# Kernel optimization log

Hardware: AMD Instinct MI355X
Metric: run time of the kernel (lower is better)

## Reference

```python
import jax, jax.numpy as jnp
import numpy as np

E = 8        # num_experts
D = 512      # embed_size
H = 8        # attention heads
HD = D // H  # head dim
B, S = 4, 1024


def setup_inputs() -> dict:
    key = jax.random.key(0)
    ks = jax.random.split(key, 16)
    sd = 0.02
    return {
        "x":  jax.random.normal(ks[0], (B, S, D), jnp.float32),
        # per-expert FFN params, stacked over expert dim
        "W1": jax.random.normal(ks[1], (E, D, 4 * D), jnp.float32) * sd,
        "b1": jnp.zeros((E, 4 * D), jnp.float32),
        "W2": jax.random.normal(ks[2], (E, 4 * D, D), jnp.float32) * sd,
        "b2": jnp.zeros((E, D), jnp.float32),
        # MultiheadAttention in_proj (split) and out_proj
        "Wq": jax.random.normal(ks[3], (D, D), jnp.float32) * sd,
        "bq": jnp.zeros((D,), jnp.float32),
        "Wk": jax.random.normal(ks[4], (D, D), jnp.float32) * sd,
        "bk": jnp.zeros((D,), jnp.float32),
        "Wv": jax.random.normal(ks[5], (D, D), jnp.float32) * sd,
        "bv": jnp.zeros((D,), jnp.float32),
        "Wo": jax.random.normal(ks[6], (D, D), jnp.float32) * sd,
        "bo": jnp.zeros((D,), jnp.float32),
        "expert_id": 3,
    }


def reference(x, W1, b1, W2, b2, Wq, bq, Wk, bk, Wv, bv, Wo, bo, expert_id):
    # --- batched per-expert FFN (fuses the Python loop over experts) ---
    # hidden: [B, E, S, 4D]
    hidden = jax.nn.relu(jnp.einsum('bsd,edf->besf', x, W1) + b1[None, :, None, :])
    eo = jnp.einsum('besf,efd->besd', hidden, W2) + b2[None, :, None, :]  # [B,E,S,D]
    eo = eo.transpose(0, 2, 1, 3)  # [B, S, E, D]

    Bs, Ss = x.shape[0], x.shape[1]
    a = eo.reshape(Bs * Ss, E, D)  # [N, E, D]; attention runs over the expert dim

    # --- MultiheadAttention (batch_first), torch semantics ---
    # NOTE: the original passes a FLOAT tril-of-ones attn_mask, which torch ADDS
    # to the scores (it does NOT mask with -inf). We reproduce that faithfully.
    q = (a @ Wq.T + bq).reshape(-1, E, H, HD).transpose(0, 2, 1, 3)  # [N,H,E,hd]
    k = (a @ Wk.T + bk).reshape(-1, E, H, HD).transpose(0, 2, 1, 3)
    v = (a @ Wv.T + bv).reshape(-1, E, H, HD).transpose(0, 2, 1, 3)

    mask = jnp.tril(jnp.ones((E, E), jnp.float32))  # additive float mask
    scores = jnp.einsum('nhed,nhfd->nhef', q, k) / jnp.sqrt(jnp.float32(HD))
    scores = scores + mask[None, None, :, :]
    attn = jax.nn.softmax(scores, axis=-1)
    ctx = jnp.einsum('nhef,nhfd->nhed', attn, v)           # [N,H,E,hd]
    ctx = ctx.transpose(0, 2, 1, 3).reshape(-1, E, D)       # [N,E,D]
    out = ctx @ Wo.T + bo                                   # [N,E,D]

    out = out.reshape(Bs, Ss, E, D)
    return out[:, :, expert_id, :]  # [B, S, D]
```

## Files before the change

kernel.cpp:

```cpp
#include <hip/hip_runtime.h>
#include <hip/hip_bf16.h>

typedef __hip_bfloat16 bf16;
typedef __attribute__((ext_vector_type(4))) float f32x4;
typedef __attribute__((ext_vector_type(8))) short s16x8;

#define N_TOK 4096
#define Dm    512
#define Fm    2048
#define Em    8

__device__ __forceinline__ float bf2f(bf16 v) { return __bfloat162float(v); }
__device__ __forceinline__ bf16  f2bf(float f) { return __float2bfloat16(f); }

#define GL16(g, l)                                                              \
  __builtin_amdgcn_global_load_lds(                                             \
      (const __attribute__((address_space(1))) void*)(g),                       \
      (__attribute__((address_space(3))) void*)(l), 16, 0, 0)

__global__ void cvt_f32_bf16(const float* __restrict__ in, bf16* __restrict__ out, int n4) {
  int i = blockIdx.x * 256 + threadIdx.x;
  if (i >= n4) return;
  float4 v = reinterpret_cast<const float4*>(in)[i];
  bf16 tmp[4] = {f2bf(v.x), f2bf(v.y), f2bf(v.z), f2bf(v.w)};
  __builtin_memcpy(out + (size_t)i * 4, tmp, 8);
}

__global__ void transpose_cvt(const float* __restrict__ in, bf16* __restrict__ out,
                              int R, int C, long inb, long outb) {
  in  += (long)blockIdx.z * inb;
  out += (long)blockIdx.z * outb;
  __shared__ float t[32][33];
  int tx = threadIdx.x & 31, ty = threadIdx.x >> 5;
  int c0 = blockIdx.x * 32, r0 = blockIdx.y * 32;
#pragma unroll
  for (int i = 0; i < 32; i += 8)
    t[ty + i][tx] = in[(long)(r0 + ty + i) * C + c0 + tx];
  __syncthreads();
#pragma unroll
  for (int i = 0; i < 32; i += 8)
    out[(long)(c0 + ty + i) * R + r0 + tx] = f2bf(t[tx][ty + i]);
}

template <bool RELU, bool OUT_BF16>
__global__ __launch_bounds__(256, 2) void gemm_bt(
    const bf16* __restrict__ A, const bf16* __restrict__ Bt, void* __restrict__ Cout,
    const float* __restrict__ bias, int M, int N, int K, int lda, int ldb, int ldc,
    long abs_, long bbs, long cbs, long biasbs, const int* __restrict__ eid,
    int eid_scale) {
  int e = blockIdx.z;
  A    += (long)e * abs_;
  Bt   += (long)e * bbs;
  bias += (long)e * biasbs;
  long coff = (long)e * cbs;
  if (eid) A += (long)(*eid) * eid_scale;

  __shared__ bf16 As[128 * 32];
  __shared__ bf16 Bs[128 * 32];

  int tid = threadIdx.x;
  int wave = tid >> 6, lane = tid & 63;
  int wm = wave >> 1, wn = wave & 1;
  int bm = blockIdx.x * 128, bn = blockIdx.y * 128;

  int srow  = lane >> 2;
  int skoff = (lane & 3) * 8;

  f32x4 acc[4][4] = {};

  const bf16* Abase = A + (long)bm * lda;
  const bf16* Bbase = Bt + (long)bn * ldb;

  for (int k0 = 0; k0 < K; k0 += 32) {
    __syncthreads();
#pragma unroll
    for (int i = 0; i < 2; i++) {
      int r = wave * 32 + i * 16 + srow;
      GL16(Abase + (long)r * lda + k0 + skoff, As + (wave * 32 + i * 16) * 32);
      GL16(Bbase + (long)r * ldb + k0 + skoff, Bs + (wave * 32 + i * 16) * 32);
    }
    __syncthreads();

    s16x8 af[4], bfr[4];
#pragma unroll
    for (int m = 0; m < 4; m++)
      af[m] = *reinterpret_cast<const s16x8*>(As + (wm * 64 + m * 16 + (lane & 15)) * 32 +
                                              (lane >> 4) * 8);
#pragma unroll
    for (int n = 0; n < 4; n++)
      bfr[n] = *reinterpret_cast<const s16x8*>(Bs + (wn * 64 + n * 16 + (lane & 15)) * 32 +
                                               (lane >> 4) * 8);
#pragma unroll
    for (int m = 0; m < 4; m++)
#pragma unroll
      for (int n = 0; n < 4; n++)
        acc[m][n] = __builtin_amdgcn_mfma_f32_16x16x32_bf16(af[m], bfr[n], acc[m][n], 0, 0, 0);
  }

  int cr = (lane >> 4) * 4, cc = lane & 15;
#pragma unroll
  for (int m = 0; m < 4; m++) {
#pragma unroll
    for (int n = 0; n < 4; n++) {
      int col  = bn + wn * 64 + n * 16 + cc;
      float bv = bias ? bias[col] : 0.0f;
#pragma unroll
      for (int r = 0; r < 4; r++) {
        int row = bm + wm * 64 + m * 16 + cr + r;
        float v = acc[m][n][r] + bv;
        if (RELU) v = fmaxf(v, 0.0f);
        long idx = coff + (long)row * ldc + col;
        if (OUT_BF16)
          ((bf16*)Cout)[idx] = f2bf(v);
        else
          ((float*)Cout)[idx] = v;
      }
    }
  }
}

__global__ __launch_bounds__(256) void attn_kernel(const float* __restrict__ q,
                                                   const bf16* __restrict__ kv,
                                                   bf16* __restrict__ ctx,
                                                   const int* __restrict__ eid) {
  int wave = threadIdx.x >> 6, lane = threadIdx.x & 63;
  int n = blockIdx.x * 4 + wave;
  int h = lane >> 3, f = lane & 7;
  int e3 = *eid;
  const bf16* kvn = kv + (long)n * Em * (2 * Dm);
  const float* qh = q + (long)n * Dm + h * 64;
  const bf16* kf = kvn + f * (2 * Dm) + h * 64;
  float s = 0.f;
#pragma unroll
  for (int j = 0; j < 64; j++) s += qh[j] * bf2f(kf[j]);
  s *= 0.125f;
  s += (f <= e3) ? 1.0f : 0.0f;
  float mx = s;
#pragma unroll
  for (int d = 1; d < 8; d <<= 1) mx = fmaxf(mx, __shfl_xor(mx, d));
  float ex = expf(s - mx);
  float sm = ex;
#pragma unroll
  for (int d = 1; d < 8; d <<= 1) sm += __shfl_xor(sm, d);
  float at = ex / sm;
  int g = f;
  float acc[8] = {0, 0, 0, 0, 0, 0, 0, 0};
#pragma unroll
  for (int f2 = 0; f2 < 8; f2++) {
    float a = __shfl(at, (h << 3) | f2);
    const bf16* vf = kvn + f2 * (2 * Dm) + Dm + h * 64 + g * 8;
#pragma unroll
    for (int j = 0; j < 8; j++) acc[j] += a * bf2f(vf[j]);
  }
  bf16 tmp[8];
#pragma unroll
  for (int j = 0; j < 8; j++) tmp[j] = f2bf(acc[j]);
  __builtin_memcpy(ctx + (long)n * Dm + h * 64 + g * 8, tmp, 16);
}

extern "C" void kernel_launch(void* const* d_in, const int* in_sizes, int n_in,
                              void* d_out, int out_size, void* d_ws, size_t ws_size,
                              hipStream_t stream) {
  const float* x  = (const float*)d_in[0];
  const float* W1 = (const float*)d_in[1];
  const float* b1 = (const float*)d_in[2];
  const float* W2 = (const float*)d_in[3];
  const float* b2 = (const float*)d_in[4];
  const float* Wq = (const float*)d_in[5];
  const float* bq = (const float*)d_in[6];
  const float* Wk = (const float*)d_in[7];
  const float* bk = (const float*)d_in[8];
  const float* Wv = (const float*)d_in[9];
  const float* bv = (const float*)d_in[10];
  const float* Wo = (const float*)d_in[11];
  const float* bo = (const float*)d_in[12];
  const int* eid  = (const int*)d_in[13];

  char* w = (char*)d_ws;
  auto alloc = [&](size_t bytes) {
    char* p = w;
    w += (bytes + 255) & ~(size_t)255;
    return p;
  };
  bf16* xb   = (bf16*)alloc((size_t)N_TOK * Dm * 2);
  bf16* W1t  = (bf16*)alloc((size_t)Em * Fm * Dm * 2);
  bf16* W2t  = (bf16*)alloc((size_t)Em * Dm * Fm * 2);
  bf16* qw   = (bf16*)alloc((size_t)Dm * Dm * 2);
  bf16* kvw  = (bf16*)alloc((size_t)2 * Dm * Dm * 2);
  bf16* ow   = (bf16*)alloc((size_t)Dm * Dm * 2);
  float* bkv = (float*)alloc((size_t)2 * Dm * 4);
  bf16* hid  = (bf16*)alloc((size_t)Em * N_TOK * Fm * 2);
  bf16* eo   = (bf16*)alloc((size_t)N_TOK * Em * Dm * 2);
  bf16* kv   = (bf16*)hid;
  float* qb  = (float*)(hid + (size_t)N_TOK * Em * 2 * Dm);
  bf16* ctxb = (bf16*)(qb + (size_t)N_TOK * Dm);

  cvt_f32_bf16<<<(N_TOK * Dm / 4 + 255) / 256, 256, 0, stream>>>(x, xb, N_TOK * Dm / 4);
  transpose_cvt<<<dim3(Fm / 32, Dm / 32, Em), 256, 0, stream>>>(
      W1, W1t, Dm, Fm, (long)Dm * Fm, (long)Fm * Dm);
  transpose_cvt<<<dim3(Dm / 32, Fm / 32, Em), 256, 0, stream>>>(
      W2, W2t, Fm, Dm, (long)Fm * Dm, (long)Dm * Fm);
  int nw4 = Dm * Dm / 4;
  cvt_f32_bf16<<<(nw4 + 255) / 256, 256, 0, stream>>>(Wq, qw, nw4);
  cvt_f32_bf16<<<(nw4 + 255) / 256, 256, 0, stream>>>(Wk, kvw, nw4);
  cvt_f32_bf16<<<(nw4 + 255) / 256, 256, 0, stream>>>(Wv, kvw + (size_t)Dm * Dm, nw4);
  cvt_f32_bf16<<<(nw4 + 255) / 256, 256, 0, stream>>>(Wo, ow, nw4);
  hipMemcpyAsync(bkv, bk, Dm * sizeof(float), hipMemcpyDeviceToDevice, stream);
  hipMemcpyAsync(bkv + Dm, bv, Dm * sizeof(float), hipMemcpyDeviceToDevice, stream);

  gemm_bt<true, true><<<dim3(N_TOK / 128, Fm / 128, Em), 256, 0, stream>>>(
      xb, W1t, hid, b1, N_TOK, Fm, Dm, Dm, Dm, Fm,
      0L, (long)Fm * Dm, (long)N_TOK * Fm, (long)Fm, nullptr, 0);
  gemm_bt<false, true><<<dim3(N_TOK / 128, Dm / 128, Em), 256, 0, stream>>>(
      hid, W2t, eo, b2, N_TOK, Dm, Fm, Fm, Fm, Em * Dm,
      (long)N_TOK * Fm, (long)Dm * Fm, (long)Dm, (long)Dm, nullptr, 0);
  gemm_bt<false, true><<<dim3(N_TOK * Em / 128, 2 * Dm / 128, 1), 256, 0, stream>>>(
      eo, kvw, kv, bkv, N_TOK * Em, 2 * Dm, Dm, Dm, Dm, 2 * Dm,
      0L, 0L, 0L, 0L, nullptr, 0);
  gemm_bt<false, false><<<dim3(N_TOK / 128, Dm / 128, 1), 256, 0, stream>>>(
      eo, qw, qb, bq, N_TOK, Dm, Dm, Em * Dm, Dm, Dm,
      0L, 0L, 0L, 0L, eid, Dm);
  attn_kernel<<<N_TOK / 4, 256, 0, stream>>>(qb, kv, ctxb, eid);
  gemm_bt<false, false><<<dim3(N_TOK / 128, Dm / 128, 1), 256, 0, stream>>>(
      ctxb, ow, (float*)d_out, bo, N_TOK, Dm, Dm, Dm, Dm, Dm,
      0L, 0L, 0L, 0L, nullptr, 0);
}
```

Before: 314.4 us.

## Add 256x256 triple-buffered GEMM with swizzled LDS and XCD-aware block mapping

```diff
diff --git a/kernel.cpp b/kernel.cpp
--- a/kernel.cpp
+++ b/kernel.cpp
@@ -40,6 +40,122 @@
 #pragma unroll
   for (int i = 0; i < 32; i += 8)
     out[(long)(c0 + ty + i) * R + r0 + tx] = f2bf(t[tx][ty + i]);
+}
+
+template <bool RELU, bool OUT_BF16>
+__global__ __launch_bounds__(512, 2) void gemm256(
+    const bf16* __restrict__ A, const bf16* __restrict__ Bt, void* __restrict__ Cout,
+    const float* __restrict__ bias, int K, int lda, int ldb, int ldc,
+    long abs_, long bbs, long cbs, long biasbs, int gx, int gy) {
+  extern __shared__ bf16 lds[];
+
+  int nwg = gridDim.x;
+  int id  = blockIdx.x;
+  int lid = (id & 7) * (nwg >> 3) + (id >> 3);
+  int per = gx * gy;
+  int e   = lid / per;
+  int rem = lid - e * per;
+  int bx  = rem % gx, by = rem / gx;
+  int bm  = bx * 256, bn = by * 256;
+
+  A    += (long)e * abs_;
+  Bt   += (long)e * bbs;
+  bias += (long)e * biasbs;
+  long coff = (long)e * cbs;
+
+  int tid  = threadIdx.x;
+  int w    = tid >> 6, lane = tid & 63;
+  int wm   = w >> 2, wn = w & 3;
+
+  int srow   = lane >> 2;
+  int schunk = (lane & 3) ^ ((lane >> 3) & 3);
+
+  const bf16* Ab = A + (long)bm * lda;
+  const bf16* Bb = Bt + (long)bn * ldb;
+
+  int nt = K >> 5;
+
+  auto issue = [&](int t) {
+    int k0 = t << 5;
+    bf16* buf = lds + (t % 3) * 16384;
+#pragma unroll
+    for (int j = 0; j < 2; ++j) {
+      int ch   = j * 8 + w;
+      int rowA = ch * 16 + srow;
+      GL16(Ab + (long)rowA * lda + k0 + schunk * 8, buf + ch * 512);
+      GL16(Bb + (long)rowA * ldb + k0 + schunk * 8, buf + 8192 + ch * 512);
+    }
+  };
+
+  f32x4 acc[8][4] = {};
+  int la = lane & 15, q = lane >> 4;
+  int slotr = q ^ ((la >> 1) & 3);
+
+  auto compute = [&](int t) {
+    const bf16* Abuf = lds + (t % 3) * 16384;
+    const bf16* Bbuf = Abuf + 8192;
+    s16x8 af[8], bfr[4];
+#pragma unroll
+    for (int m = 0; m < 8; ++m) {
+      int r = wm * 128 + m * 16 + la;
+      af[m] = *reinterpret_cast<const s16x8*>(Abuf + r * 32 + slotr * 8);
+    }
+#pragma unroll
+    for (int n = 0; n < 4; ++n) {
+      int r = wn * 64 + n * 16 + la;
+      bfr[n] = *reinterpret_cast<const s16x8*>(Bbuf + r * 32 + slotr * 8);
+    }
+    __builtin_amdgcn_s_setprio(1);
+#pragma unroll
+    for (int m = 0; m < 8; ++m)
+#pragma unroll
+      for (int n = 0; n < 4; ++n)
+        acc[m][n] = __builtin_amdgcn_mfma_f32_16x16x32_bf16(bfr[n], af[m], acc[m][n], 0, 0, 0);
+    __builtin_amdgcn_s_setprio(0);
+  };
+
+  issue(0);
+  issue(1);
+
+  for (int t = 0; t < nt - 1; ++t) {
+    asm volatile("s_waitcnt vmcnt(4)" ::: "memory");
+    __builtin_amdgcn_s_barrier();
+    asm volatile("" ::: "memory");
+    __builtin_amdgcn_sched_barrier(0);
+    if (t + 2 < nt) issue(t + 2);
+    compute(t);
+    __builtin_amdgcn_sched_barrier(0);
+  }
+  asm volatile("s_waitcnt vmcnt(0)" ::: "memory");
+  __builtin_amdgcn_s_barrier();
+  asm volatile("" ::: "memory");
+  __builtin_amdgcn_sched_barrier(0);
+  compute(nt - 1);
+
+  int nbase0 = bn + wn * 64 + q * 4;
+#pragma unroll
+  for (int m = 0; m < 8; ++m) {
+    int gm = bm + wm * 128 + m * 16 + la;
+#pragma unroll
+    for (int n = 0; n < 4; ++n) {
+      int gn = nbase0 + n * 16;
+      float4 b4 = *reinterpret_cast<const float4*>(bias + gn);
+      float v0 = acc[m][n][0] + b4.x, v1 = acc[m][n][1] + b4.y;
+      float v2 = acc[m][n][2] + b4.z, v3 = acc[m][n][3] + b4.w;
+      if (RELU) {
+        v0 = fmaxf(v0, 0.f); v1 = fmaxf(v1, 0.f);
+        v2 = fmaxf(v2, 0.f); v3 = fmaxf(v3, 0.f);
+      }
+      long idx = coff + (long)gm * ldc + gn;
+      if (OUT_BF16) {
+        bf16 tmp[4] = {f2bf(v0), f2bf(v1), f2bf(v2), f2bf(v3)};
+        __builtin_memcpy((bf16*)Cout + idx, tmp, 8);
+      } else {
+        float tmp[4] = {v0, v1, v2, v3};
+        __builtin_memcpy((float*)Cout + idx, tmp, 16);
+      }
+    }
+  }
 }
 
 template <bool RELU, bool OUT_BF16>
@@ -195,6 +311,11 @@
   float* qb  = (float*)(hid + (size_t)N_TOK * Em * 2 * Dm);
   bf16* ctxb = (bf16*)(qb + (size_t)N_TOK * Dm);
 
+  hipFuncSetAttribute(reinterpret_cast<const void*>(gemm256<true, true>),
+                      hipFuncAttributeMaxDynamicSharedMemorySize, 98304);
+  hipFuncSetAttribute(reinterpret_cast<const void*>(gemm256<false, true>),
+                      hipFuncAttributeMaxDynamicSharedMemorySize, 98304);
+
   cvt_f32_bf16<<<(N_TOK * Dm / 4 + 255) / 256, 256, 0, stream>>>(x, xb, N_TOK * Dm / 4);
   transpose_cvt<<<dim3(Fm / 32, Dm / 32, Em), 256, 0, stream>>>(
       W1, W1t, Dm, Fm, (long)Dm * Fm, (long)Fm * Dm);
@@ -208,15 +329,15 @@
   hipMemcpyAsync(bkv, bk, Dm * sizeof(float), hipMemcpyDeviceToDevice, stream);
   hipMemcpyAsync(bkv + Dm, bv, Dm * sizeof(float), hipMemcpyDeviceToDevice, stream);
 
-  gemm_bt<true, true><<<dim3(N_TOK / 128, Fm / 128, Em), 256, 0, stream>>>(
-      xb, W1t, hid, b1, N_TOK, Fm, Dm, Dm, Dm, Fm,
-      0L, (long)Fm * Dm, (long)N_TOK * Fm, (long)Fm, nullptr, 0);
-  gemm_bt<false, true><<<dim3(N_TOK / 128, Dm / 128, Em), 256, 0, stream>>>(
-      hid, W2t, eo, b2, N_TOK, Dm, Fm, Fm, Fm, Em * Dm,
-      (long)N_TOK * Fm, (long)Dm * Fm, (long)Dm, (long)Dm, nullptr, 0);
-  gemm_bt<false, true><<<dim3(N_TOK * Em / 128, 2 * Dm / 128, 1), 256, 0, stream>>>(
-      eo, kvw, kv, bkv, N_TOK * Em, 2 * Dm, Dm, Dm, Dm, 2 * Dm,
-      0L, 0L, 0L, 0L, nullptr, 0);
+  gemm256<true, true><<<16 * 8 * Em, 512, 98304, stream>>>(
+      xb, W1t, hid, b1, Dm, Dm, Dm, Fm,
+      0L, (long)Fm * Dm, (long)N_TOK * Fm, (long)Fm, 16, 8);
+  gemm256<false, true><<<16 * 2 * Em, 512, 98304, stream>>>(
+      hid, W2t, eo, b2, Fm, Fm, Fm, Em * Dm,
+      (long)N_TOK * Fm, (long)Dm * Fm, (long)Dm, (long)Dm, 16, 2);
+  gemm256<false, true><<<128 * 4, 512, 98304, stream>>>(
+      eo, kvw, kv, bkv, Dm, Dm, Dm, 2 * Dm,
+      0L, 0L, 0L, 0L, 128, 4);
   gemm_bt<false, false><<<dim3(N_TOK / 128, Dm / 128, 1), 256, 0, stream>>>(
       eo, qw, qb, bq, N_TOK, Dm, Dm, Em * Dm, Dm, Dm,
       0L, 0L, 0L, 0L, eid, Dm);
```

Result: slower. 321.6 us (+2.3%).

## Add swizzled BK=64 GEMM with XCD-aware block remap for FFN and KV projections

Applied to the files above, without the earlier changes.

```diff
diff --git a/kernel.cpp b/kernel.cpp
--- a/kernel.cpp
+++ b/kernel.cpp
@@ -40,6 +40,94 @@
 #pragma unroll
   for (int i = 0; i < 32; i += 8)
     out[(long)(c0 + ty + i) * R + r0 + tx] = f2bf(t[tx][ty + i]);
+}
+
+template <bool RELU, bool OUT_BF16>
+__global__ __launch_bounds__(256, 4) void gemm128(
+    const bf16* __restrict__ A, const bf16* __restrict__ Bt, void* __restrict__ Cout,
+    const float* __restrict__ bias, int K, int lda, int ldb, int ldc,
+    long abs_, long bbs, long cbs, long biasbs, int gx, int gy,
+    const int* __restrict__ eid, int eid_scale) {
+  __shared__ bf16 As[128 * 64];
+  __shared__ bf16 Bs[128 * 64];
+
+  int nwg = gridDim.x;
+  int id  = blockIdx.x;
+  int lid = (id & 7) * (nwg >> 3) + (id >> 3);
+  int per = gx * gy;
+  int e   = lid / per;
+  int rem = lid - e * per;
+  int bx  = rem % gx, by = rem / gx;
+  int bm  = bx * 128, bn = by * 128;
+
+  A    += (long)e * abs_;
+  Bt   += (long)e * bbs;
+  bias += (long)e * biasbs;
+  long coff = (long)e * cbs;
+  if (eid) A += (long)(*eid) * eid_scale;
+
+  int tid = threadIdx.x, wv = tid >> 6, lane = tid & 63;
+  int wm = wv >> 1, wn = wv & 1;
+
+  const bf16* Ab = A + (long)bm * lda;
+  const bf16* Bb = Bt + (long)bn * ldb;
+
+  f32x4 acc[4][4] = {};
+  int la = lane & 15, q = lane >> 4;
+  int srow_lo = lane >> 3;
+
+  for (int k0 = 0; k0 < K; k0 += 64) {
+    __syncthreads();
+#pragma unroll
+    for (int j = 0; j < 4; ++j) {
+      int r = (wv * 4 + j) * 8 + srow_lo;
+      int c = (lane & 7) ^ (r & 7);
+      GL16(Ab + (long)r * lda + k0 + c * 8, As + (wv * 4 + j) * 512);
+      GL16(Bb + (long)r * ldb + k0 + c * 8, Bs + (wv * 4 + j) * 512);
+    }
+    __syncthreads();
+
+#pragma unroll
+    for (int kk = 0; kk < 2; ++kk) {
+      int ps = (kk * 4 + q) ^ (la & 7);
+      s16x8 af[4], bfr[4];
+#pragma unroll
+      for (int m = 0; m < 4; ++m)
+        af[m] = *reinterpret_cast<const s16x8*>(As + (wm * 64 + m * 16 + la) * 64 + ps * 8);
+#pragma unroll
+      for (int n = 0; n < 4; ++n)
+        bfr[n] = *reinterpret_cast<const s16x8*>(Bs + (wn * 64 + n * 16 + la) * 64 + ps * 8);
+#pragma unroll
+      for (int m = 0; m < 4; ++m)
+#pragma unroll
+        for (int n = 0; n < 4; ++n)
+          acc[m][n] = __builtin_amdgcn_mfma_f32_16x16x32_bf16(bfr[n], af[m], acc[m][n], 0, 0, 0);
+    }
+  }
+
+#pragma unroll
+  for (int m = 0; m < 4; ++m) {
+    int gm = bm + wm * 64 + m * 16 + la;
+#pragma unroll
+    for (int n = 0; n < 4; ++n) {
+      int gn = bn + wn * 64 + n * 16 + q * 4;
+      float4 b4 = *reinterpret_cast<const float4*>(bias + gn);
+      float v0 = acc[m][n][0] + b4.x, v1 = acc[m][n][1] + b4.y;
+      float v2 = acc[m][n][2] + b4.z, v3 = acc[m][n][3] + b4.w;
+      if (RELU) {
+        v0 = fmaxf(v0, 0.f); v1 = fmaxf(v1, 0.f);
+        v2 = fmaxf(v2, 0.f); v3 = fmaxf(v3, 0.f);
+      }
+      long idx = coff + (long)gm * ldc + gn;
+      if (OUT_BF16) {
+        bf16 tmp[4] = {f2bf(v0), f2bf(v1), f2bf(v2), f2bf(v3)};
+        __builtin_memcpy((bf16*)Cout + idx, tmp, 8);
+      } else {
+        float tmp[4] = {v0, v1, v2, v3};
+        __builtin_memcpy((float*)Cout + idx, tmp, 16);
+      }
+    }
+  }
 }
 
 template <bool RELU, bool OUT_BF16>
@@ -208,15 +296,15 @@
   hipMemcpyAsync(bkv, bk, Dm * sizeof(float), hipMemcpyDeviceToDevice, stream);
   hipMemcpyAsync(bkv + Dm, bv, Dm * sizeof(float), hipMemcpyDeviceToDevice, stream);
 
-  gemm_bt<true, true><<<dim3(N_TOK / 128, Fm / 128, Em), 256, 0, stream>>>(
-      xb, W1t, hid, b1, N_TOK, Fm, Dm, Dm, Dm, Fm,
-      0L, (long)Fm * Dm, (long)N_TOK * Fm, (long)Fm, nullptr, 0);
-  gemm_bt<false, true><<<dim3(N_TOK / 128, Dm / 128, Em), 256, 0, stream>>>(
-      hid, W2t, eo, b2, N_TOK, Dm, Fm, Fm, Fm, Em * Dm,
-      (long)N_TOK * Fm, (long)Dm * Fm, (long)Dm, (long)Dm, nullptr, 0);
-  gemm_bt<false, true><<<dim3(N_TOK * Em / 128, 2 * Dm / 128, 1), 256, 0, stream>>>(
-      eo, kvw, kv, bkv, N_TOK * Em, 2 * Dm, Dm, Dm, Dm, 2 * Dm,
-      0L, 0L, 0L, 0L, nullptr, 0);
+  gemm128<true, true><<<32 * 16 * Em, 256, 0, stream>>>(
+      xb, W1t, hid, b1, Dm, Dm, Dm, Fm,
+      0L, (long)Fm * Dm, (long)N_TOK * Fm, (long)Fm, 32, 16, nullptr, 0);
+  gemm128<false, true><<<32 * 4 * Em, 256, 0, stream>>>(
+      hid, W2t, eo, b2, Fm, Fm, Fm, Em * Dm,
+      (long)N_TOK * Fm, (long)Dm * Fm, (long)Dm, (long)Dm, 32, 4, nullptr, 0);
+  gemm128<false, true><<<256 * 8, 256, 0, stream>>>(
+      eo, kvw, kv, bkv, Dm, Dm, Dm, 2 * Dm,
+      0L, 0L, 0L, 0L, 256, 8, nullptr, 0);
   gemm_bt<false, false><<<dim3(N_TOK / 128, Dm / 128, 1), 256, 0, stream>>>(
       eo, qw, qb, bq, N_TOK, Dm, Dm, Em * Dm, Dm, Dm,
       0L, 0L, 0L, 0L, eid, Dm);
```

Result: slower. 330.5 us (+5.1%).
